# Optimization experiments

Hardware: AMD Instinct MI355X
Metric: run time of the kernel (lower is better)

## Reference

```python
import jax, jax.numpy as jnp
import numpy as np


def _sqdist(x1, x2):
    # squared euclidean distance matrix, [n1, n2]
    n1 = jnp.sum(x1 * x1, axis=-1)[:, None]
    n2 = jnp.sum(x2 * x2, axis=-1)[None, :]
    d2 = n1 + n2 - 2.0 * (x1 @ x2.T)
    return jnp.maximum(d2, 0.0)


def _rbf(x1, x2, raw_length_scale, raw_variance):
    ls = jax.nn.softplus(raw_length_scale)[0]
    var = jax.nn.softplus(raw_variance)[0]
    return var * jnp.exp(-0.5 * _sqdist(x1, x2) / (ls * ls))


def setup_inputs() -> dict:
    key = jax.random.key(0)
    k1, k2, k3 = jax.random.split(key, 3)
    N_TRAIN, N_TEST, D = 4096, 8192, 8
    return {
        "x_train": jax.random.uniform(k1, (N_TRAIN, D), dtype=jnp.float32),
        "y_train": jax.random.normal(k2, (N_TRAIN,), dtype=jnp.float32),
        "w_train": jnp.ones((N_TRAIN,), dtype=jnp.float32),
        "x_test": jax.random.uniform(k3, (N_TEST, D), dtype=jnp.float32),
        "raw_length_scale": jnp.array([0.6931471824645996], dtype=jnp.float32),
        "raw_variance": jnp.array([0.6931471824645996], dtype=jnp.float32),
        "raw_noise_var": jnp.array([0.1], dtype=jnp.float32),
    }


def reference(x_train, y_train, w_train, x_test,
              raw_length_scale, raw_variance, raw_noise_var):
    n = x_train.shape[0]
    noise_var = jax.nn.softplus(raw_noise_var)[0]
    eye = jnp.eye(n, dtype=x_train.dtype)

    K = _rbf(x_train, x_train, raw_length_scale, raw_variance) + (noise_var + 1e-6) * eye

    # off-diagonal entries scaled by w_i * w_j, diagonal kept as-is
    non_diag = 1.0 - eye
    weight = w_train[:, None] * w_train[None, :]
    weighted_K = K * (non_diag * weight + eye)

    K_s = _rbf(x_train, x_test, raw_length_scale, raw_variance)
    weighted_K_s = w_train[:, None] * K_s  # diag(w) @ K_s

    K_ss = _rbf(x_test, x_test, raw_length_scale, raw_variance) \
        + 1e-6 * jnp.eye(x_test.shape[0], dtype=x_test.dtype)

    L = jnp.linalg.cholesky(weighted_K)
    alpha = jax.scipy.linalg.cho_solve((L, True), y_train[:, None])  # [n, 1]
    mu = (weighted_K_s.T @ alpha)[:, 0]  # [n_test]

    v = jax.scipy.linalg.solve_triangular(L, weighted_K_s, lower=True)  # [n, n_test]
    cov = K_ss - v.T @ v
    return mu, cov
```

## Files before the change

kernel.cpp:

```cpp
#include <hip/hip_runtime.h>
#include <math.h>

#define NT 4096
#define MT 8192
#define NB 128
#define NBLK 32
#define TBM 128
#define TBN 64
#define TBK 32
#define SRPB 64

typedef unsigned short u16;
typedef short v8s __attribute__((ext_vector_type(8)));
typedef float v4f __attribute__((ext_vector_type(4)));

__device__ __forceinline__ float bf2f(u16 h) {
  return __uint_as_float(((unsigned)h) << 16);
}
__device__ __forceinline__ u16 f2bf(float x) {
  unsigned u = __float_as_uint(x);
  u += 0x7fffu + ((u >> 16) & 1u);
  return (u16)(u >> 16);
}
__device__ __forceinline__ void split1(float x, u16& h, u16& l) {
  h = f2bf(x);
  l = f2bf(x - bf2f(h));
}
__device__ __forceinline__ float softplusf(float x) { return log1pf(expf(x)); }

__device__ __forceinline__ void load8bf(const u16* __restrict__ p, float* f) {
  ushort4 u0 = *(const ushort4*)p;
  ushort4 u1 = *(const ushort4*)(p + 4);
  f[0] = bf2f(u0.x); f[1] = bf2f(u0.y); f[2] = bf2f(u0.z); f[3] = bf2f(u0.w);
  f[4] = bf2f(u1.x); f[5] = bf2f(u1.y); f[6] = bf2f(u1.z); f[7] = bf2f(u1.w);
}

__device__ __forceinline__ float getsc(const void* p, int f32) {
  return f32 ? *(const float*)p : bf2f(*(const u16*)p);
}
__device__ __forceinline__ float getel(const void* p, int i, int f32) {
  return f32 ? ((const float*)p)[i] : bf2f(((const u16*)p)[i]);
}
__device__ __forceinline__ void load_pt(const void* xb, int idx, int f32, float* f) {
  if (f32) {
    const float4* q = (const float4*)xb;
    float4 a = q[idx * 2], b = q[idx * 2 + 1];
    f[0] = a.x; f[1] = a.y; f[2] = a.z; f[3] = a.w;
    f[4] = b.x; f[5] = b.y; f[6] = b.z; f[7] = b.w;
  } else {
    load8bf((const u16*)xb + idx * 8, f);
  }
}

__global__ void detect_dtype(const u16* __restrict__ xt, int* __restrict__ flag) {
  if (threadIdx.x == 0) {
    int f = 0;
    for (int i = 0; i < 32; i++) if (xt[i] >= 0x4000) f = 1;
    flag[0] = f;
  }
}

__global__ void build_K(const void* __restrict__ xt, const void* __restrict__ w,
                        const void* __restrict__ rls, const void* __restrict__ rvar,
                        const void* __restrict__ rnv, float* __restrict__ K,
                        const int* __restrict__ flag) {
  int f32 = flag[0];
  int j = blockIdx.x * 16 + threadIdx.x;
  int i = blockIdx.y * 16 + threadIdx.y;
  float ls  = softplusf(getsc(rls, f32));
  float var = softplusf(getsc(rvar, f32));
  float cc  = -0.5f / (ls * ls);
  float v;
  if (i == j) {
    v = var + softplusf(getsc(rnv, f32)) + 1e-6f;
  } else {
    float a[8], b[8];
    load_pt(xt, i, f32, a);
    load_pt(xt, j, f32, b);
    float d = 0.f;
#pragma unroll
    for (int q = 0; q < 8; q++) { float t = a[q] - b[q]; d += t * t; }
    v = var * expf(cc * d) * getel(w, i, f32) * getel(w, j, f32);
  }
  K[(size_t)i * NT + j] = v;
}

__global__ void build_Kst(const void* __restrict__ xt, const void* __restrict__ xs,
                          const void* __restrict__ w, const void* __restrict__ rls,
                          const void* __restrict__ rvar,
                          u16* __restrict__ hi, u16* __restrict__ lo,
                          const int* __restrict__ flag) {
  int f32 = flag[0];
  int i = blockIdx.x * 16 + threadIdx.x;
  int j = blockIdx.y * 16 + threadIdx.y;
  float ls  = softplusf(getsc(rls, f32));
  float var = softplusf(getsc(rvar, f32));
  float cc  = -0.5f / (ls * ls);
  float a[8], b[8];
  load_pt(xt, i, f32, a);
  load_pt(xs, j, f32, b);
  float d = 0.f;
#pragma unroll
  for (int q = 0; q < 8; q++) { float t = a[q] - b[q]; d += t * t; }
  float v = getel(w, i, f32) * var * expf(cc * d);
  size_t o = (size_t)j * NT + i;
  u16 h, l; split1(v, h, l);
  hi[o] = h; lo[o] = l;
}

__global__ void __launch_bounds__(256) potrf_invert(float* __restrict__ Kg,
                                                    float* __restrict__ Wall, int kb) {
  __shared__ float At[NB * NB];
  __shared__ float Wv[NB * NB];
  int tid = threadIdx.x;
  int r0 = kb * NB;
  for (int idx = tid; idx < NB * NB; idx += 256) {
    int k = idx >> 7, i = idx & 127;
    At[idx] = Kg[(size_t)(r0 + k) * NT + r0 + i];
    Wv[idx] = (k == i) ? 1.f : 0.f;
  }
  __syncthreads();
  for (int j = 0; j < NB; j++) {
    float inv = 1.0f / At[j * NB + j];
    int nel = (NB - 1 - j) << 7;
    for (int idx = tid; idx < nel; idx += 256) {
      int k = j + 1 + (idx >> 7);
      int i = idx & 127;
      if (i >= k) At[k * NB + i] -= At[j * NB + i] * (At[j * NB + k] * inv);
    }
    __syncthreads();
  }
  for (int t = 0; t < NB; t++) {
    float invd = 1.0f / At[t * NB + t];
    int nel = (NB - 1 - t) << 7;
    for (int idx = tid; idx < nel; idx += 256) {
      int i = t + 1 + (idx >> 7);
      int c = idx & 127;
      Wv[i * NB + c] -= (At[t * NB + i] * invd) * Wv[t * NB + c];
    }
    __syncthreads();
  }
  for (int idx = tid; idx < NB * NB; idx += 256) {
    int k = idx >> 7, i = idx & 127;
    if (i >= k) {
      float s = sqrtf(At[k * NB + k]);
      Kg[(size_t)(r0 + i) * NT + r0 + k] = (i == k) ? s : At[idx] / s;
    }
  }
  float* Wg = Wall + (size_t)kb * NB * NB;
  for (int idx = tid; idx < NB * NB; idx += 256) {
    int i = idx >> 7;
    Wg[idx] = Wv[idx] / sqrtf(At[i * NB + i]);
  }
}

__global__ void copy_panel(const float* __restrict__ Kg, float* __restrict__ S,
                           int t0, int rows, int kb) {
  int idx = blockIdx.x * 256 + threadIdx.x;
  if (idx < rows * NB) {
    int r = idx >> 7, c = idx & 127;
    S[idx] = Kg[(size_t)(t0 + r) * NT + kb * NB + c];
  }
}

template<int SUB, int SYRK>
__global__ void __launch_bounds__(256) gemm_nt(const float* __restrict__ A, int lda,
                                               const float* __restrict__ B, int ldb,
                                               float* __restrict__ C, int ldc, int Kdim) {
  int c0 = blockIdx.x * TBN;
  int r0 = blockIdx.y * TBM;
  if (SYRK && c0 > r0 + TBM - 1) return;
  __shared__ float As[TBK][TBM + 4];
  __shared__ float Bs[TBK][TBN + 4];
  int tid = threadIdx.x;
  int tx = tid & 15, ty = tid >> 4;
  float acc[8][4];
#pragma unroll
  for (int r = 0; r < 8; r++)
#pragma unroll
    for (int c = 0; c < 4; c++) acc[r][c] = 0.f;

  int am = tid & 127, ah = tid >> 7;
  int bc = tid & 63,  bh = tid >> 6;

  for (int kt = 0; kt < Kdim; kt += TBK) {
#pragma unroll
    for (int q = 0; q < 4; q++) {
      int s = ah * 4 + q;
      float4 v = *(const float4*)&A[(size_t)(r0 + am) * lda + kt + s * 4];
      As[s * 4 + 0][am] = v.x; As[s * 4 + 1][am] = v.y;
      As[s * 4 + 2][am] = v.z; As[s * 4 + 3][am] = v.w;
    }
#pragma unroll
    for (int q = 0; q < 2; q++) {
      int s = bh * 2 + q;
      float4 v = *(const float4*)&B[(size_t)(c0 + bc) * ldb + kt + s * 4];
      Bs[s * 4 + 0][bc] = v.x; Bs[s * 4 + 1][bc] = v.y;
      Bs[s * 4 + 2][bc] = v.z; Bs[s * 4 + 3][bc] = v.w;
    }
    __syncthreads();
#pragma unroll
    for (int k = 0; k < TBK; k++) {
      float a[8], b[4];
      *(float4*)&a[0] = *(const float4*)&As[k][ty * 8];
      *(float4*)&a[4] = *(const float4*)&As[k][ty * 8 + 4];
      *(float4*)&b[0] = *(const float4*)&Bs[k][tx * 4];
#pragma unroll
      for (int r = 0; r < 8; r++)
#pragma unroll
        for (int c = 0; c < 4; c++) acc[r][c] += a[r] * b[c];
    }
    __syncthreads();
  }
#pragma unroll
  for (int r = 0; r < 8; r++) {
    float* cp = &C[(size_t)(r0 + ty * 8 + r) * ldc + c0 + tx * 4];
    if (SUB) {
      float4 o = *(const float4*)cp;
      o.x -= acc[r][0]; o.y -= acc[r][1]; o.z -= acc[r][2]; o.w -= acc[r][3];
      *(float4*)cp = o;
    } else {
      float4 o; o.x = acc[r][0]; o.y = acc[r][1]; o.z = acc[r][2]; o.w = acc[r][3];
      *(float4*)cp = o;
    }
  }
}

__global__ void init_r(const void* __restrict__ y, float* __restrict__ r,
                       const int* __restrict__ flag) {
  int i = blockIdx.x * 256 + threadIdx.x;
  r[i] = getel(y, i, flag[0]);
}

__global__ void __launch_bounds__(256) fwd_step(const float* __restrict__ Lg,
                                                const float* __restrict__ Wall,
                                                float* __restrict__ r,
                                                float* __restrict__ z, int kb) {
  __shared__ float ts[NB];
  __shared__ float part[256];
  int tid = threadIdx.x;
  int r0 = kb * NB;
  {
    int row = tid >> 1, half = tid & 1;
    const float* Wr = Wall + (size_t)kb * NB * NB + row * NB + half * 64;
    const float* rv = r + r0 + half * 64;
    float acc = 0.f;
#pragma unroll
    for (int c = 0; c < 64; c += 4) {
      float4 wv = *(const float4*)&Wr[c];
      float4 xv = *(const float4*)&rv[c];
      acc += wv.x * xv.x + wv.y * xv.y + wv.z * xv.z + wv.w * xv.w;
    }
    part[tid] = acc;
    __syncthreads();
    if (half == 0) ts[row] = part[tid] + part[tid + 1];
    __syncthreads();
  }
  if (blockIdx.x == 0) {
    if (tid < NB) z[r0 + tid] = ts[tid];
    return;
  }
  int base = r0 + NB + (blockIdx.x - 1) * SRPB;
  int wv_ = tid >> 6, lane = tid & 63;
  for (int rr = wv_; rr < SRPB; rr += 4) {
    int row = base + rr;
    const float* Lr = Lg + (size_t)row * NT + r0;
    float acc = Lr[lane] * ts[lane] + Lr[lane + 64] * ts[lane + 64];
#pragma unroll
    for (int off = 32; off > 0; off >>= 1) acc += __shfl_down(acc, off, 64);
    if (lane == 0) r[row] -= acc;
  }
}

__global__ void __launch_bounds__(256) bwd_step(const float* __restrict__ Lg,
                                                const float* __restrict__ Wall,
                                                float* __restrict__ z,
                                                float* __restrict__ a, int kb) {
  __shared__ float ts[NB];
  __shared__ float part[256];
  int tid = threadIdx.x;
  int r0 = kb * NB;
  {
    int col = tid & 127, half = tid >> 7;
    const float* Wb = Wall + (size_t)kb * NB * NB;
    float acc = 0.f;
#pragma unroll 4
    for (int rr = half * 64; rr < half * 64 + 64; rr++)
      acc += Wb[rr * NB + col] * z[r0 + rr];
    part[tid] = acc;
    __syncthreads();
    if (half == 0) ts[col] = part[tid] + part[tid + 128];
    __syncthreads();
  }
  if (blockIdx.x == 0) {
    if (tid < NB) a[r0 + tid] = ts[tid];
    return;
  }
  int cb = blockIdx.x - 1;
  int col = cb * NB + (tid & 127);
  int half = tid >> 7;
  float acc = 0.f;
#pragma unroll 4
  for (int jr = half * 64; jr < half * 64 + 64; jr++)
    acc += Lg[(size_t)(r0 + jr) * NT + col] * ts[jr];
  part[tid] = acc;
  __syncthreads();
  if (half == 0) z[col] -= part[tid] + part[tid + 128];
}

__global__ void conv_W(const float* __restrict__ src, u16* __restrict__ hi,
                       u16* __restrict__ lo) {
  int idx = (blockIdx.x * 256 + threadIdx.x) * 4;
  float4 v = *(const float4*)&src[idx];
  ushort4 h, l;
  split1(v.x, h.x, l.x); split1(v.y, h.y, l.y);
  split1(v.z, h.z, l.z); split1(v.w, h.w, l.w);
  *(ushort4*)&hi[idx] = h;
  *(ushort4*)&lo[idx] = l;
}

__global__ void __launch_bounds__(256) mu_dot(const u16* __restrict__ hi,
                                              const u16* __restrict__ lo,
                                              const float* __restrict__ alpha,
                                              float* __restrict__ mu) {
  int lane = threadIdx.x & 63, wv = threadIdx.x >> 6;
  int j = blockIdx.x * 4 + wv;
  const u16* ph = hi + (size_t)j * NT;
  const u16* pl = lo + (size_t)j * NT;
  float s = 0.f;
  for (int c = lane * 4; c < NT; c += 256) {
    ushort4 h = *(const ushort4*)&ph[c];
    ushort4 l = *(const ushort4*)&pl[c];
    float4 a = *(const float4*)&alpha[c];
    s += (bf2f(h.x) + bf2f(l.x)) * a.x + (bf2f(h.y) + bf2f(l.y)) * a.y
       + (bf2f(h.z) + bf2f(l.z)) * a.z + (bf2f(h.w) + bf2f(l.w)) * a.w;
  }
#pragma unroll
  for (int off = 32; off > 0; off >>= 1) s += __shfl_down(s, off, 64);
  if (lane == 0) mu[j] = s;
}

template<int MODE, int BF32>
__global__ void __launch_bounds__(256) mm_bf16(
    const u16* __restrict__ Ah, const u16* __restrict__ Al, int lda,
    const u16* __restrict__ Bh, const u16* __restrict__ Bl,
    const float* __restrict__ Bf, int ldb,
    u16* __restrict__ Chi, u16* __restrict__ Clo, float* __restrict__ Cf,
    int ldc, int Kdim,
    const void* __restrict__ xs, const void* __restrict__ rls,
    const void* __restrict__ rvar, const int* __restrict__ flag) {
  int c0 = blockIdx.x * 128;
  int r0 = blockIdx.y * 128;
  if (MODE == 2 && r0 < c0) return;
  __shared__ u16 L[4][128 * 64];
  int tid = threadIdx.x;
  int lane = tid & 63, wv = tid >> 6;
  int wr = wv >> 1, wc = wv & 1;
  int lr = lane & 15, lk = lane >> 4;

  v4f acc[4][4];
  v4f zero = {0.f, 0.f, 0.f, 0.f};
#pragma unroll
  for (int mi = 0; mi < 4; mi++)
#pragma unroll
    for (int ni = 0; ni < 4; ni++) acc[mi][ni] = zero;

  for (int kt = 0; kt < Kdim; kt += 64) {
    int4 rga[8], rgb[8];
#pragma unroll
    for (int p = 0; p < 4; p++) {
      int ch = p * 256 + tid;
      int row = ch >> 3, sl = ch & 7;
      size_t o = (size_t)(r0 + row) * lda + kt + sl * 8;
      rga[p]     = *(const int4*)(Ah + o);
      rga[p + 4] = *(const int4*)(Al + o);
    }
    if (BF32 == 0) {
#pragma unroll
      for (int p = 0; p < 4; p++) {
        int ch = p * 256 + tid;
        int row = ch >> 3, sl = ch & 7;
        size_t o = (size_t)(c0 + row) * ldb + kt + sl * 8;
        rgb[p]     = *(const int4*)(Bh + o);
        rgb[p + 4] = *(const int4*)(Bl + o);
      }
    } else {
#pragma unroll
      for (int p = 0; p < 8; p++) {
        int ch = p * 256 + tid;
        int row = ch >> 4, f4 = ch & 15;
        rgb[p] = *(const int4*)(Bf + (size_t)(c0 + row) * ldb + kt + f4 * 4);
      }
    }
    __syncthreads();
#pragma unroll
    for (int p = 0; p < 4; p++) {
      int ch = p * 256 + tid;
      int row = ch >> 3, sl = ch & 7;
      int off = row * 64 + ((sl ^ (row & 7)) * 8);
      *(int4*)&L[0][off] = rga[p];
      *(int4*)&L[1][off] = rga[p + 4];
      if (BF32 == 0) {
        *(int4*)&L[2][off] = rgb[p];
        *(int4*)&L[3][off] = rgb[p + 4];
      }
    }
    if (BF32 == 1) {
#pragma unroll
      for (int p = 0; p < 8; p++) {
        int ch = p * 256 + tid;
        int row = ch >> 4, f4 = ch & 15;
        const float* v = (const float*)&rgb[p];
        ushort4 h, l;
        split1(v[0], h.x, l.x); split1(v[1], h.y, l.y);
        split1(v[2], h.z, l.z); split1(v[3], h.w, l.w);
        int sl = f4 >> 1, half = f4 & 1;
        int off = row * 64 + ((sl ^ (row & 7)) * 8) + half * 4;
        *(ushort4*)&L[2][off] = h;
        *(ushort4*)&L[3][off] = l;
      }
    }
    __syncthreads();
#pragma unroll
    for (int ks = 0; ks < 2; ks++) {
      v8s afh[4], afl[4], bfh[4], bfl[4];
#pragma unroll
      for (int mi = 0; mi < 4; mi++) {
        int row = wr * 64 + mi * 16 + lr;
        int sl = (ks * 4 + lk) ^ (row & 7);
        afh[mi] = *(const v8s*)&L[0][row * 64 + sl * 8];
        afl[mi] = *(const v8s*)&L[1][row * 64 + sl * 8];
      }
#pragma unroll
      for (int ni = 0; ni < 4; ni++) {
        int row = wc * 64 + ni * 16 + lr;
        int sl = (ks * 4 + lk) ^ (row & 7);
        bfh[ni] = *(const v8s*)&L[2][row * 64 + sl * 8];
        bfl[ni] = *(const v8s*)&L[3][row * 64 + sl * 8];
      }
#pragma unroll
      for (int mi = 0; mi < 4; mi++)
#pragma unroll
        for (int ni = 0; ni < 4; ni++) {
          acc[mi][ni] = __builtin_amdgcn_mfma_f32_16x16x32_bf16(afh[mi], bfh[ni], acc[mi][ni], 0, 0, 0);
          acc[mi][ni] = __builtin_amdgcn_mfma_f32_16x16x32_bf16(afh[mi], bfl[ni], acc[mi][ni], 0, 0, 0);
          acc[mi][ni] = __builtin_amdgcn_mfma_f32_16x16x32_bf16(afl[mi], bfh[ni], acc[mi][ni], 0, 0, 0);
        }
    }
  }

  if (MODE == 2) {
    int f32 = flag[0];
    float ls  = softplusf(getsc(rls, f32));
    float var = softplusf(getsc(rvar, f32));
    float cc  = -0.5f / (ls * ls);
#pragma unroll
    for (int mi = 0; mi < 4; mi++) {
#pragma unroll
      for (int r = 0; r < 4; r++) {
        int grow = r0 + wr * 64 + mi * 16 + lk * 4 + r;
        float xr[8];
        load_pt(xs, grow, f32, xr);
#pragma unroll
        for (int ni = 0; ni < 4; ni++) {
          int gcol = c0 + wc * 64 + ni * 16 + lr;
          float xc[8];
          load_pt(xs, gcol, f32, xc);
          float d = 0.f;
#pragma unroll
          for (int q = 0; q < 8; q++) { float t = xr[q] - xc[q]; d += t * t; }
          float kss = var * expf(cc * d);
          if (grow == gcol) kss += 1e-6f;
          float ov = kss - acc[mi][ni][r];
          Cf[(size_t)grow * ldc + gcol] = ov;
          if (grow > gcol) Cf[(size_t)gcol * ldc + grow] = ov;
        }
      }
    }
  } else {
#pragma unroll
    for (int mi = 0; mi < 4; mi++) {
#pragma unroll
      for (int r = 0; r < 4; r++) {
        int grow = r0 + wr * 64 + mi * 16 + lk * 4 + r;
#pragma unroll
        for (int ni = 0; ni < 4; ni++) {
          int gcol = c0 + wc * 64 + ni * 16 + lr;
          size_t o = (size_t)grow * ldc + gcol;
          float nv;
          if (MODE == 0) {
            nv = acc[mi][ni][r];
          } else {
            nv = (bf2f(Chi[o]) + bf2f(Clo[o])) - acc[mi][ni][r];
          }
          u16 h, l; split1(nv, h, l);
          Chi[o] = h; Clo[o] = l;
        }
      }
    }
  }
}

extern "C" void kernel_launch(void* const* d_in, const int* in_sizes, int n_in,
                              void* d_out, int out_size, void* d_ws, size_t ws_size,
                              hipStream_t stream) {
  (void)in_sizes; (void)n_in; (void)out_size; (void)ws_size;
  const void* xt  = d_in[0];
  const void* y   = d_in[1];
  const void* w   = d_in[2];
  const void* xs  = d_in[3];
  const void* rls = d_in[4];
  const void* rva = d_in[5];
  const void* rnv = d_in[6];

  float* mu_out  = (float*)d_out;
  float* cov_out = mu_out + MT;

  float* Kf   = (float*)d_ws;
  float* Wall = Kf + (size_t)NT * NT;
  float* S    = Wall + (size_t)NBLK * NB * NB;
  float* rbuf = S + (size_t)(NT - NB) * NB;
  float* zbuf = rbuf + NT;
  float* abuf = zbuf + NT;
  int*   flag = (int*)(abuf + NT);
  u16* Whi  = (u16*)(flag + 4);
  u16* Wlo  = Whi + (size_t)NBLK * NB * NB;
  u16* Vthi = Wlo + (size_t)NBLK * NB * NB;
  u16* Vtlo = Vthi + (size_t)MT * NT;

  detect_dtype<<<1, 64, 0, stream>>>((const u16*)xt, flag);
  build_K<<<dim3(NT / 16, NT / 16), dim3(16, 16), 0, stream>>>(xt, w, rls, rva, rnv, Kf, flag);
  build_Kst<<<dim3(NT / 16, MT / 16), dim3(16, 16), 0, stream>>>(xt, xs, w, rls, rva,
                                                                 Vthi, Vtlo, flag);

  for (int kb = 0; kb < NBLK; kb++) {
    potrf_invert<<<1, 256, 0, stream>>>(Kf, Wall, kb);
    int t0 = (kb + 1) * NB;
    int rows = NT - t0;
    if (rows > 0) {
      copy_panel<<<(rows * NB) / 256, 256, 0, stream>>>(Kf, S, t0, rows, kb);
      gemm_nt<0, 0><<<dim3(NB / TBN, rows / TBM), 256, 0, stream>>>(
          S, NB, Wall + (size_t)kb * NB * NB, NB,
          Kf + (size_t)t0 * NT + kb * NB, NT, NB);
      gemm_nt<1, 1><<<dim3(rows / TBN, rows / TBM), 256, 0, stream>>>(
          Kf + (size_t)t0 * NT + kb * NB, NT,
          Kf + (size_t)t0 * NT + kb * NB, NT,
          Kf + (size_t)t0 * NT + t0, NT, NB);
    }
  }

  conv_W<<<(NBLK * NB * NB) / 1024, 256, 0, stream>>>(Wall, Whi, Wlo);

  init_r<<<NT / 256, 256, 0, stream>>>(y, rbuf, flag);
  for (int kb = 0; kb < NBLK; kb++) {
    int nupd = (NT - (kb + 1) * NB) / SRPB;
    fwd_step<<<1 + nupd, 256, 0, stream>>>(Kf, Wall, rbuf, zbuf, kb);
  }
  for (int kb = NBLK - 1; kb >= 0; kb--) {
    bwd_step<<<1 + kb, 256, 0, stream>>>(Kf, Wall, zbuf, abuf, kb);
  }

  mu_dot<<<MT / 4, 256, 0, stream>>>(Vthi, Vtlo, abuf, mu_out);

  for (int kb = 0; kb < NBLK; kb++) {
    mm_bf16<0, 0><<<dim3(1, MT / 128), 256, 0, stream>>>(
        Vthi + kb * NB, Vtlo + kb * NB, NT,
        Whi + (size_t)kb * NB * NB, Wlo + (size_t)kb * NB * NB, nullptr, NB,
        Vthi + kb * NB, Vtlo + kb * NB, nullptr, NT, NB,
        nullptr, nullptr, nullptr, nullptr);
    int t0 = (kb + 1) * NB;
    int rows = NT - t0;
    if (rows > 0) {
      mm_bf16<1, 1><<<dim3(rows / 128, MT / 128), 256, 0, stream>>>(
          Vthi + kb * NB, Vtlo + kb * NB, NT,
          nullptr, nullptr, Kf + (size_t)t0 * NT + kb * NB, NT,
          Vthi + t0, Vtlo + t0, nullptr, NT, NB,
          nullptr, nullptr, nullptr, nullptr);
    }
  }

  mm_bf16<2, 0><<<dim3(MT / 128, MT / 128), 256, 0, stream>>>(
      Vthi, Vtlo, NT, Vthi, Vtlo, nullptr, NT,
      nullptr, nullptr, cov_out, MT, NT,
      xs, rls, rva, flag);
}
```

Measured before the change: 29.35 ms.

## Fuse blocked Cholesky, solves and TRSM into persistent kernels with grid barriers

Replaces the roughly 200 per-block kernel launches for Cholesky factorization, triangular solves and the V triangular solve with two persistent kernels of 256 blocks. The blocks synchronize through an atomic-counter grid barrier. Each block redundantly factors and inverts the 128x128 diagonal tile, so the separate potrf launch and panel copy go away. The W bf16 split is also folded into the factorization step. This removes launch overhead and serial single-block phases, at the cost of redundant diagonal work, spin-barrier latency, and a deadlock risk if not all 256 blocks are co-resident.

```diff
diff --git a/kernel.cpp b/kernel.cpp
--- a/kernel.cpp
+++ b/kernel.cpp
@@ -5,10 +5,7 @@
 #define MT 8192
 #define NB 128
 #define NBLK 32
-#define TBM 128
-#define TBN 64
-#define TBK 32
-#define SRPB 64
+#define CGRID 256
 
 typedef unsigned short u16;
 typedef short v8s __attribute__((ext_vector_type(8)));
@@ -52,11 +49,32 @@
   }
 }
 
-__global__ void detect_dtype(const u16* __restrict__ xt, int* __restrict__ flag) {
+__device__ __forceinline__ void gbar(unsigned* bar) {
+  __syncthreads();
+  if (threadIdx.x == 0) {
+    __threadfence();
+    unsigned g = __hip_atomic_load(bar + 1, __ATOMIC_RELAXED, __HIP_MEMORY_SCOPE_AGENT);
+    unsigned n = __hip_atomic_fetch_add(bar, 1u, __ATOMIC_ACQ_REL, __HIP_MEMORY_SCOPE_AGENT);
+    if (n == (unsigned)(CGRID - 1)) {
+      __hip_atomic_store(bar, 0u, __ATOMIC_RELAXED, __HIP_MEMORY_SCOPE_AGENT);
+      __hip_atomic_fetch_add(bar + 1, 1u, __ATOMIC_RELEASE, __HIP_MEMORY_SCOPE_AGENT);
+    } else {
+      while (__hip_atomic_load(bar + 1, __ATOMIC_ACQUIRE, __HIP_MEMORY_SCOPE_AGENT) == g)
+        __builtin_amdgcn_s_sleep(2);
+    }
+    __threadfence();
+  }
+  __syncthreads();
+}
+
+__global__ void detect_dtype(const u16* __restrict__ xt, int* __restrict__ flag,
+                             unsigned* __restrict__ bar) {
   if (threadIdx.x == 0) {
     int f = 0;
     for (int i = 0; i < 32; i++) if (xt[i] >= 0x4000) f = 1;
     flag[0] = f;
+    bar[0] = 0u;
+    bar[1] = 0u;
   }
 }
 
@@ -108,236 +126,392 @@
   hi[o] = h; lo[o] = l;
 }
 
-__global__ void __launch_bounds__(256) potrf_invert(float* __restrict__ Kg,
-                                                    float* __restrict__ Wall, int kb) {
+__global__ void __launch_bounds__(256) coop_chol(
+    float* __restrict__ Kf, float* __restrict__ Wall,
+    u16* __restrict__ Whi, u16* __restrict__ Wlo,
+    const void* __restrict__ y, float* __restrict__ rbuf,
+    float* __restrict__ zbuf, float* __restrict__ abuf,
+    const int* __restrict__ flag, unsigned* __restrict__ bar) {
   __shared__ float At[NB * NB];
-  __shared__ float Wv[NB * NB];
-  int tid = threadIdx.x;
-  int r0 = kb * NB;
-  for (int idx = tid; idx < NB * NB; idx += 256) {
-    int k = idx >> 7, i = idx & 127;
-    At[idx] = Kg[(size_t)(r0 + k) * NT + r0 + i];
-    Wv[idx] = (k == i) ? 1.f : 0.f;
-  }
-  __syncthreads();
-  for (int j = 0; j < NB; j++) {
-    float inv = 1.0f / At[j * NB + j];
-    int nel = (NB - 1 - j) << 7;
-    for (int idx = tid; idx < nel; idx += 256) {
-      int k = j + 1 + (idx >> 7);
-      int i = idx & 127;
-      if (i >= k) At[k * NB + i] -= At[j * NB + i] * (At[j * NB + k] * inv);
+  __shared__ float Wv[NB * 130];
+  __shared__ float tsv[NB];
+  __shared__ float part[256];
+  int tid = threadIdx.x, bid = blockIdx.x;
+
+  for (int kb = 0; kb < NBLK; kb++) {
+    int r0 = kb * NB;
+    int t0 = r0 + NB;
+    int rowsK = NT - t0;
+
+    for (int idx = tid; idx < NB * NB; idx += 256) {
+      int k = idx >> 7, i = idx & 127;
+      At[idx] = Kf[(size_t)(r0 + k) * NT + r0 + i];
+      Wv[k * 130 + i] = (k == i) ? 1.f : 0.f;
     }
     __syncthreads();
-  }
-  for (int t = 0; t < NB; t++) {
-    float invd = 1.0f / At[t * NB + t];
-    int nel = (NB - 1 - t) << 7;
-    for (int idx = tid; idx < nel; idx += 256) {
-      int i = t + 1 + (idx >> 7);
-      int c = idx & 127;
-      Wv[i * NB + c] -= (At[t * NB + i] * invd) * Wv[t * NB + c];
+    for (int j = 0; j < NB; j++) {
+      float inv = 1.0f / At[j * NB + j];
+      int nel = (NB - 1 - j) << 7;
+      for (int idx = tid; idx < nel; idx += 256) {
+        int k = j + 1 + (idx >> 7);
+        int i = idx & 127;
+        if (i >= k) At[k * NB + i] -= At[j * NB + i] * (At[j * NB + k] * inv);
+      }
+      __syncthreads();
+    }
+    for (int t = 0; t < NB; t++) {
+      float invd = 1.0f / At[t * NB + t];
+      int nel = (NB - 1 - t) << 7;
+      for (int idx = tid; idx < nel; idx += 256) {
+        int i = t + 1 + (idx >> 7);
+        int c = idx & 127;
+        Wv[i * 130 + c] -= (At[t * NB + i] * invd) * Wv[t * 130 + c];
+      }
+      __syncthreads();
+    }
+    for (int idx = tid; idx < NB * NB; idx += 256) {
+      int i = idx >> 7, c = idx & 127;
+      Wv[i * 130 + c] *= 1.0f / sqrtf(At[i * NB + i]);
     }
     __syncthreads();
-  }
-  for (int idx = tid; idx < NB * NB; idx += 256) {
-    int k = idx >> 7, i = idx & 127;
-    if (i >= k) {
-      float s = sqrtf(At[k * NB + k]);
-      Kg[(size_t)(r0 + i) * NT + r0 + k] = (i == k) ? s : At[idx] / s;
-    }
-  }
-  float* Wg = Wall + (size_t)kb * NB * NB;
-  for (int idx = tid; idx < NB * NB; idx += 256) {
-    int i = idx >> 7;
-    Wg[idx] = Wv[idx] / sqrtf(At[i * NB + i]);
-  }
-}
-
-__global__ void copy_panel(const float* __restrict__ Kg, float* __restrict__ S,
-                           int t0, int rows, int kb) {
-  int idx = blockIdx.x * 256 + threadIdx.x;
-  if (idx < rows * NB) {
-    int r = idx >> 7, c = idx & 127;
-    S[idx] = Kg[(size_t)(t0 + r) * NT + kb * NB + c];
-  }
-}
-
-template<int SUB, int SYRK>
-__global__ void __launch_bounds__(256) gemm_nt(const float* __restrict__ A, int lda,
-                                               const float* __restrict__ B, int ldb,
-                                               float* __restrict__ C, int ldc, int Kdim) {
-  int c0 = blockIdx.x * TBN;
-  int r0 = blockIdx.y * TBM;
-  if (SYRK && c0 > r0 + TBM - 1) return;
-  __shared__ float As[TBK][TBM + 4];
-  __shared__ float Bs[TBK][TBN + 4];
-  int tid = threadIdx.x;
-  int tx = tid & 15, ty = tid >> 4;
-  float acc[8][4];
-#pragma unroll
-  for (int r = 0; r < 8; r++)
-#pragma unroll
-    for (int c = 0; c < 4; c++) acc[r][c] = 0.f;
-
-  int am = tid & 127, ah = tid >> 7;
-  int bc = tid & 63,  bh = tid >> 6;
-
-  for (int kt = 0; kt < Kdim; kt += TBK) {
-#pragma unroll
-    for (int q = 0; q < 4; q++) {
-      int s = ah * 4 + q;
-      float4 v = *(const float4*)&A[(size_t)(r0 + am) * lda + kt + s * 4];
-      As[s * 4 + 0][am] = v.x; As[s * 4 + 1][am] = v.y;
-      As[s * 4 + 2][am] = v.z; As[s * 4 + 3][am] = v.w;
-    }
-#pragma unroll
-    for (int q = 0; q < 2; q++) {
-      int s = bh * 2 + q;
-      float4 v = *(const float4*)&B[(size_t)(c0 + bc) * ldb + kt + s * 4];
-      Bs[s * 4 + 0][bc] = v.x; Bs[s * 4 + 1][bc] = v.y;
-      Bs[s * 4 + 2][bc] = v.z; Bs[s * 4 + 3][bc] = v.w;
+    if (bid == 0) {
+      for (int idx = tid; idx < NB * NB; idx += 256) {
+        int k = idx >> 7, i = idx & 127;
+        if (i >= k) {
+          float s = sqrtf(At[k * NB + k]);
+          Kf[(size_t)(r0 + i) * NT + r0 + k] = (i == k) ? s : At[k * NB + i] / s;
+        }
+        float wv = Wv[k * 130 + i];
+        Wall[(size_t)kb * NB * NB + idx] = wv;
+        u16 h, l; split1(wv, h, l);
+        Whi[(size_t)kb * NB * NB + idx] = h;
+        Wlo[(size_t)kb * NB * NB + idx] = l;
+      }
     }
     __syncthreads();
-#pragma unroll
-    for (int k = 0; k < TBK; k++) {
-      float a[8], b[4];
-      *(float4*)&a[0] = *(const float4*)&As[k][ty * 8];
-      *(float4*)&a[4] = *(const float4*)&As[k][ty * 8 + 4];
-      *(float4*)&b[0] = *(const float4*)&Bs[k][tx * 4];
+
+    if (rowsK > 0 && bid < (rowsK >> 6)) {
+      int m0 = t0 + bid * 64;
+      for (int ch = tid; ch < 64 * 32; ch += 256) {
+        int row = ch >> 5, c4 = ch & 31;
+        float4 v = *(const float4*)&Kf[(size_t)(m0 + row) * NT + r0 + c4 * 4];
+        At[(c4 * 4 + 0) * 68 + row] = v.x; At[(c4 * 4 + 1) * 68 + row] = v.y;
+        At[(c4 * 4 + 2) * 68 + row] = v.z; At[(c4 * 4 + 3) * 68 + row] = v.w;
+      }
+      __syncthreads();
+      float pa[8][4];
 #pragma unroll
       for (int r = 0; r < 8; r++)
 #pragma unroll
-        for (int c = 0; c < 4; c++) acc[r][c] += a[r] * b[c];
-    }
-    __syncthreads();
-  }
-#pragma unroll
-  for (int r = 0; r < 8; r++) {
-    float* cp = &C[(size_t)(r0 + ty * 8 + r) * ldc + c0 + tx * 4];
-    if (SUB) {
-      float4 o = *(const float4*)cp;
-      o.x -= acc[r][0]; o.y -= acc[r][1]; o.z -= acc[r][2]; o.w -= acc[r][3];
-      *(float4*)cp = o;
-    } else {
-      float4 o; o.x = acc[r][0]; o.y = acc[r][1]; o.z = acc[r][2]; o.w = acc[r][3];
-      *(float4*)cp = o;
-    }
-  }
-}
-
-__global__ void init_r(const void* __restrict__ y, float* __restrict__ r,
-                       const int* __restrict__ flag) {
-  int i = blockIdx.x * 256 + threadIdx.x;
-  r[i] = getel(y, i, flag[0]);
-}
-
-__global__ void __launch_bounds__(256) fwd_step(const float* __restrict__ Lg,
-                                                const float* __restrict__ Wall,
-                                                float* __restrict__ r,
-                                                float* __restrict__ z, int kb) {
-  __shared__ float ts[NB];
-  __shared__ float part[256];
-  int tid = threadIdx.x;
-  int r0 = kb * NB;
-  {
-    int row = tid >> 1, half = tid & 1;
-    const float* Wr = Wall + (size_t)kb * NB * NB + row * NB + half * 64;
-    const float* rv = r + r0 + half * 64;
-    float acc = 0.f;
-#pragma unroll
-    for (int c = 0; c < 64; c += 4) {
-      float4 wv = *(const float4*)&Wr[c];
-      float4 xv = *(const float4*)&rv[c];
-      acc += wv.x * xv.x + wv.y * xv.y + wv.z * xv.z + wv.w * xv.w;
-    }
-    part[tid] = acc;
-    __syncthreads();
-    if (half == 0) ts[row] = part[tid] + part[tid + 1];
-    __syncthreads();
-  }
-  if (blockIdx.x == 0) {
-    if (tid < NB) z[r0 + tid] = ts[tid];
-    return;
-  }
-  int base = r0 + NB + (blockIdx.x - 1) * SRPB;
-  int wv_ = tid >> 6, lane = tid & 63;
-  for (int rr = wv_; rr < SRPB; rr += 4) {
-    int row = base + rr;
-    const float* Lr = Lg + (size_t)row * NT + r0;
-    float acc = Lr[lane] * ts[lane] + Lr[lane + 64] * ts[lane + 64];
-#pragma unroll
-    for (int off = 32; off > 0; off >>= 1) acc += __shfl_down(acc, off, 64);
-    if (lane == 0) r[row] -= acc;
-  }
-}
-
-__global__ void __launch_bounds__(256) bwd_step(const float* __restrict__ Lg,
-                                                const float* __restrict__ Wall,
-                                                float* __restrict__ z,
-                                                float* __restrict__ a, int kb) {
-  __shared__ float ts[NB];
-  __shared__ float part[256];
-  int tid = threadIdx.x;
-  int r0 = kb * NB;
-  {
-    int col = tid & 127, half = tid >> 7;
-    const float* Wb = Wall + (size_t)kb * NB * NB;
-    float acc = 0.f;
+        for (int c = 0; c < 4; c++) pa[r][c] = 0.f;
+      int rr0 = (tid >> 5) * 8, cc0 = (tid & 31) * 4;
+      for (int k = 0; k < NB; k++) {
+        float a0[8], b0[4];
+        *(float4*)&a0[0] = *(const float4*)&At[k * 68 + rr0];
+        *(float4*)&a0[4] = *(const float4*)&At[k * 68 + rr0 + 4];
+        b0[0] = Wv[(cc0 + 0) * 130 + k]; b0[1] = Wv[(cc0 + 1) * 130 + k];
+        b0[2] = Wv[(cc0 + 2) * 130 + k]; b0[3] = Wv[(cc0 + 3) * 130 + k];
+#pragma unroll
+        for (int r = 0; r < 8; r++)
+#pragma unroll
+          for (int c = 0; c < 4; c++) pa[r][c] += a0[r] * b0[c];
+      }
+#pragma unroll
+      for (int r = 0; r < 8; r++) {
+        float4 o; o.x = pa[r][0]; o.y = pa[r][1]; o.z = pa[r][2]; o.w = pa[r][3];
+        *(float4*)&Kf[(size_t)(m0 + rr0 + r) * NT + r0 + cc0] = o;
+      }
+    }
+    gbar(bar);
+
+    if (rowsK > 0) {
+      int nmT = rowsK >> 7, nnT = rowsK >> 6;
+      int ntile = nmT * nnT;
+      for (int ti = bid; ti < ntile; ti += CGRID) {
+        int m = ti / nnT, n = ti % nnT;
+        int m0 = t0 + m * 128, n0 = t0 + n * 64;
+        if (n0 > m0 + 127) continue;
+        __syncthreads();
+        for (int ch = tid; ch < 128 * 32; ch += 256) {
+          int row = ch >> 5, c4 = ch & 31;
+          float4 v = *(const float4*)&Kf[(size_t)(m0 + row) * NT + r0 + c4 * 4];
+          At[(c4 * 4 + 0) * 128 + row] = v.x; At[(c4 * 4 + 1) * 128 + row] = v.y;
+          At[(c4 * 4 + 2) * 128 + row] = v.z; At[(c4 * 4 + 3) * 128 + row] = v.w;
+        }
+        for (int ch = tid; ch < 64 * 32; ch += 256) {
+          int nn_ = ch >> 5, c4 = ch & 31;
+          float4 v = *(const float4*)&Kf[(size_t)(n0 + nn_) * NT + r0 + c4 * 4];
+          Wv[(c4 * 4 + 0) * 68 + nn_] = v.x; Wv[(c4 * 4 + 1) * 68 + nn_] = v.y;
+          Wv[(c4 * 4 + 2) * 68 + nn_] = v.z; Wv[(c4 * 4 + 3) * 68 + nn_] = v.w;
+        }
+        __syncthreads();
+        float ac[8][4];
+#pragma unroll
+        for (int r = 0; r < 8; r++)
+#pragma unroll
+          for (int c = 0; c < 4; c++) ac[r][c] = 0.f;
+        int ty = tid >> 4, tx = tid & 15;
+        for (int k = 0; k < 128; k++) {
+          float a0[8], b0[4];
+          *(float4*)&a0[0] = *(const float4*)&At[k * 128 + ty * 8];
+          *(float4*)&a0[4] = *(const float4*)&At[k * 128 + ty * 8 + 4];
+          *(float4*)&b0[0] = *(const float4*)&Wv[k * 68 + tx * 4];
+#pragma unroll
+          for (int r = 0; r < 8; r++)
+#pragma unroll
+            for (int c = 0; c < 4; c++) ac[r][c] += a0[r] * b0[c];
+        }
+#pragma unroll
+        for (int r = 0; r < 8; r++) {
+          float* cp = &Kf[(size_t)(m0 + ty * 8 + r) * NT + n0 + tx * 4];
+          float4 o = *(const float4*)cp;
+          o.x -= ac[r][0]; o.y -= ac[r][1]; o.z -= ac[r][2]; o.w -= ac[r][3];
+          *(float4*)cp = o;
+        }
+      }
+    }
+    gbar(bar);
+  }
+
+  int f32 = flag[0];
+  for (int i = bid * 256 + tid; i < NT; i += CGRID * 256) rbuf[i] = getel(y, i, f32);
+  gbar(bar);
+
+  for (int kb = 0; kb < NBLK; kb++) {
+    int r0 = kb * NB;
+    {
+      int row = tid >> 1, half = tid & 1;
+      const float* Wr = Wall + (size_t)kb * NB * NB + row * NB + half * 64;
+      const float* rv = rbuf + r0 + half * 64;
+      float acc = 0.f;
+#pragma unroll
+      for (int c = 0; c < 64; c += 4) {
+        float4 wv4 = *(const float4*)&Wr[c];
+        float4 xv = *(const float4*)&rv[c];
+        acc += wv4.x * xv.x + wv4.y * xv.y + wv4.z * xv.z + wv4.w * xv.w;
+      }
+      part[tid] = acc;
+      __syncthreads();
+      if (half == 0) tsv[row] = part[tid] + part[tid + 1];
+      __syncthreads();
+    }
+    if (bid == 0 && tid < NB) zbuf[r0 + tid] = tsv[tid];
+    int t0s = r0 + NB;
+    int nst = (NT - t0s) >> 6;
+    if (bid < nst) {
+      int base = t0s + bid * 64;
+      int wv_ = tid >> 6, lane = tid & 63;
+      for (int rr = wv_; rr < 64; rr += 4) {
+        int row = base + rr;
+        const float* Lr = Kf + (size_t)row * NT + r0;
+        float acc = Lr[lane] * tsv[lane] + Lr[lane + 64] * tsv[lane + 64];
+#pragma unroll
+        for (int off = 32; off > 0; off >>= 1) acc += __shfl_down(acc, off, 64);
+        if (lane == 0) rbuf[row] -= acc;
+      }
+    }
+    gbar(bar);
+  }
+
+  for (int kb = NBLK - 1; kb >= 0; kb--) {
+    int r0 = kb * NB;
+    {
+      int col = tid & 127, half = tid >> 7;
+      const float* Wb = Wall + (size_t)kb * NB * NB;
+      float acc = 0.f;
 #pragma unroll 4
-    for (int rr = half * 64; rr < half * 64 + 64; rr++)
-      acc += Wb[rr * NB + col] * z[r0 + rr];
-    part[tid] = acc;
-    __syncthreads();
-    if (half == 0) ts[col] = part[tid] + part[tid + 128];
-    __syncthreads();
-  }
-  if (blockIdx.x == 0) {
-    if (tid < NB) a[r0 + tid] = ts[tid];
-    return;
-  }
-  int cb = blockIdx.x - 1;
-  int col = cb * NB + (tid & 127);
-  int half = tid >> 7;
-  float acc = 0.f;
+      for (int rr = half * 64; rr < half * 64 + 64; rr++)
+        acc += Wb[rr * NB + col] * zbuf[r0 + rr];
+      part[tid] = acc;
+      __syncthreads();
+      if (half == 0) tsv[col] = part[tid] + part[tid + 128];
+      __syncthreads();
+    }
+    if (bid == 0 && tid < NB) abuf[r0 + tid] = tsv[tid];
+    if (bid < kb) {
+      int col = bid * NB + (tid & 127);
+      int half = tid >> 7;
+      float acc = 0.f;
 #pragma unroll 4
-  for (int jr = half * 64; jr < half * 64 + 64; jr++)
-    acc += Lg[(size_t)(r0 + jr) * NT + col] * ts[jr];
-  part[tid] = acc;
-  __syncthreads();
-  if (half == 0) z[col] -= part[tid] + part[tid + 128];
-}
-
-__global__ void conv_W(const float* __restrict__ src, u16* __restrict__ hi,
-                       u16* __restrict__ lo) {
-  int idx = (blockIdx.x * 256 + threadIdx.x) * 4;
-  float4 v = *(const float4*)&src[idx];
-  ushort4 h, l;
-  split1(v.x, h.x, l.x); split1(v.y, h.y, l.y);
-  split1(v.z, h.z, l.z); split1(v.w, h.w, l.w);
-  *(ushort4*)&hi[idx] = h;
-  *(ushort4*)&lo[idx] = l;
-}
-
-__global__ void __launch_bounds__(256) mu_dot(const u16* __restrict__ hi,
-                                              const u16* __restrict__ lo,
-                                              const float* __restrict__ alpha,
-                                              float* __restrict__ mu) {
-  int lane = threadIdx.x & 63, wv = threadIdx.x >> 6;
-  int j = blockIdx.x * 4 + wv;
-  const u16* ph = hi + (size_t)j * NT;
-  const u16* pl = lo + (size_t)j * NT;
-  float s = 0.f;
-  for (int c = lane * 4; c < NT; c += 256) {
-    ushort4 h = *(const ushort4*)&ph[c];
-    ushort4 l = *(const ushort4*)&pl[c];
-    float4 a = *(const float4*)&alpha[c];
-    s += (bf2f(h.x) + bf2f(l.x)) * a.x + (bf2f(h.y) + bf2f(l.y)) * a.y
-       + (bf2f(h.z) + bf2f(l.z)) * a.z + (bf2f(h.w) + bf2f(l.w)) * a.w;
-  }
-#pragma unroll
-  for (int off = 32; off > 0; off >>= 1) s += __shfl_down(s, off, 64);
-  if (lane == 0) mu[j] = s;
+      for (int jr = half * 64; jr < half * 64 + 64; jr++)
+        acc += Kf[(size_t)(r0 + jr) * NT + col] * tsv[jr];
+      part[tid] = acc;
+      __syncthreads();
+      if (half == 0) zbuf[col] -= part[tid] + part[tid + 128];
+    }
+    gbar(bar);
+  }
+}
+
+__device__ __forceinline__ void mfma_tile(const u16* __restrict__ LAh, const u16* __restrict__ LAl,
+                                          const u16* __restrict__ LBh, const u16* __restrict__ LBl,
+                                          v4f acc[4][4], int wr, int wc, int lr, int lk) {
+#pragma unroll
+  for (int ks = 0; ks < 2; ks++) {
+    v8s afh[4], afl[4], bfh[4], bfl[4];
+#pragma unroll
+    for (int mi = 0; mi < 4; mi++) {
+      int row = wr * 64 + mi * 16 + lr;
+      int sl = (ks * 4 + lk) ^ (row & 7);
+      afh[mi] = *(const v8s*)&LAh[row * 64 + sl * 8];
+      afl[mi] = *(const v8s*)&LAl[row * 64 + sl * 8];
+    }
+#pragma unroll
+    for (int ni = 0; ni < 4; ni++) {
+      int row = wc * 64 + ni * 16 + lr;
+      int sl = (ks * 4 + lk) ^ (row & 7);
+      bfh[ni] = *(const v8s*)&LBh[row * 64 + sl * 8];
+      bfl[ni] = *(const v8s*)&LBl[row * 64 + sl * 8];
+    }
+#pragma unroll
+    for (int mi = 0; mi < 4; mi++)
+#pragma unroll
+      for (int ni = 0; ni < 4; ni++) {
+        acc[mi][ni] = __builtin_amdgcn_mfma_f32_16x16x32_bf16(afh[mi], bfh[ni], acc[mi][ni], 0, 0, 0);
+        acc[mi][ni] = __builtin_amdgcn_mfma_f32_16x16x32_bf16(afh[mi], bfl[ni], acc[mi][ni], 0, 0, 0);
+        acc[mi][ni] = __builtin_amdgcn_mfma_f32_16x16x32_bf16(afl[mi], bfh[ni], acc[mi][ni], 0, 0, 0);
+      }
+  }
+}
+
+__global__ void __launch_bounds__(512) coop_trsm(
+    u16* __restrict__ Vthi, u16* __restrict__ Vtlo,
+    const u16* __restrict__ Whi, const u16* __restrict__ Wlo,
+    const float* __restrict__ Kf, const float* __restrict__ alpha,
+    float* __restrict__ mu, unsigned* __restrict__ bar) {
+  __shared__ u16 LAh[256 * 64], LAl[256 * 64];
+  __shared__ u16 LBh[128 * 64], LBl[128 * 64];
+  int tid = threadIdx.x, bid = blockIdx.x;
+  int lane = tid & 63, wv = tid >> 6;
+
+  for (int j = bid * 8 + wv; j < MT; j += CGRID * 8) {
+    const u16* ph = Vthi + (size_t)j * NT;
+    const u16* pl = Vtlo + (size_t)j * NT;
+    float s = 0.f;
+    for (int c = lane * 4; c < NT; c += 256) {
+      ushort4 h = *(const ushort4*)&ph[c];
+      ushort4 l = *(const ushort4*)&pl[c];
+      float4 a = *(const float4*)&alpha[c];
+      s += (bf2f(h.x) + bf2f(l.x)) * a.x + (bf2f(h.y) + bf2f(l.y)) * a.y
+         + (bf2f(h.z) + bf2f(l.z)) * a.z + (bf2f(h.w) + bf2f(l.w)) * a.w;
+    }
+#pragma unroll
+    for (int off = 32; off > 0; off >>= 1) s += __shfl_down(s, off, 64);
+    if (lane == 0) mu[j] = s;
+  }
+  gbar(bar);
+
+  int wr = wv >> 1, wc = wv & 1;
+  int lr = lane & 15, lk = lane >> 4;
+  v4f zero = {0.f, 0.f, 0.f, 0.f};
+
+  for (int kb = 0; kb < NBLK; kb++) {
+    int r0 = kb * NB;
+    if (bid < MT / 256) {
+      int m0 = bid * 256;
+      v4f acc[4][4];
+#pragma unroll
+      for (int mi = 0; mi < 4; mi++)
+#pragma unroll
+        for (int ni = 0; ni < 4; ni++) acc[mi][ni] = zero;
+      for (int kt = 0; kt < 2; kt++) {
+        int k0 = r0 + kt * 64;
+        __syncthreads();
+#pragma unroll
+        for (int p = 0; p < 4; p++) {
+          int ch = p * 512 + tid;
+          int row = ch >> 3, sl = ch & 7;
+          size_t o = (size_t)(m0 + row) * NT + k0 + sl * 8;
+          int off = row * 64 + ((sl ^ (row & 7)) * 8);
+          *(int4*)&LAh[off] = *(const int4*)(Vthi + o);
+          *(int4*)&LAl[off] = *(const int4*)(Vtlo + o);
+        }
+#pragma unroll
+        for (int p = 0; p < 2; p++) {
+          int ch = p * 512 + tid;
+          int row = ch >> 3, sl = ch & 7;
+          size_t o = (size_t)kb * NB * NB + row * NB + kt * 64 + sl * 8;
+          int off = row * 64 + ((sl ^ (row & 7)) * 8);
+          *(int4*)&LBh[off] = *(const int4*)(Whi + o);
+          *(int4*)&LBl[off] = *(const int4*)(Wlo + o);
+        }
+        __syncthreads();
+        mfma_tile(LAh, LAl, LBh, LBl, acc, wr, wc, lr, lk);
+      }
+#pragma unroll
+      for (int mi = 0; mi < 4; mi++)
+#pragma unroll
+        for (int r = 0; r < 4; r++) {
+          int grow = m0 + wr * 64 + mi * 16 + lk * 4 + r;
+#pragma unroll
+          for (int ni = 0; ni < 4; ni++) {
+            int gcol = r0 + wc * 64 + ni * 16 + lr;
+            size_t o = (size_t)grow * NT + gcol;
+            u16 h, l; split1(acc[mi][ni][r], h, l);
+            Vthi[o] = h; Vtlo[o] = l;
+          }
+        }
+    }
+    gbar(bar);
+
+    int t0 = (kb + 1) * NB, rowsT = NT - t0;
+    if (rowsT > 0) {
+      int nn = rowsT >> 7;
+      int ntile = (MT / 256) * nn;
+      for (int ti = bid; ti < ntile; ti += CGRID) {
+        int m = ti % (MT / 256), n = ti / (MT / 256);
+        int m0 = m * 256, n0 = t0 + n * 128;
+        v4f acc[4][4];
+#pragma unroll
+        for (int mi = 0; mi < 4; mi++)
+#pragma unroll
+          for (int ni = 0; ni < 4; ni++) acc[mi][ni] = zero;
+        for (int kt = 0; kt < 2; kt++) {
+          int k0 = r0 + kt * 64;
+          __syncthreads();
+#pragma unroll
+          for (int p = 0; p < 4; p++) {
+            int ch = p * 512 + tid;
+            int row = ch >> 3, sl = ch & 7;
+            size_t o = (size_t)(m0 + row) * NT + k0 + sl * 8;
+            int off = row * 64 + ((sl ^ (row & 7)) * 8);
+            *(int4*)&LAh[off] = *(const int4*)(Vthi + o);
+            *(int4*)&LAl[off] = *(const int4*)(Vtlo + o);
+          }
+#pragma unroll
+          for (int p = 0; p < 4; p++) {
+            int ch = p * 512 + tid;
+            int row = ch >> 4, f4 = ch & 15;
+            float4 v = *(const float4*)&Kf[(size_t)(n0 + row) * NT + k0 + f4 * 4];
+            ushort4 h, l;
+            split1(v.x, h.x, l.x); split1(v.y, h.y, l.y);
+            split1(v.z, h.z, l.z); split1(v.w, h.w, l.w);
+            int sl = f4 >> 1, half = f4 & 1;
+            int off = row * 64 + ((sl ^ (row & 7)) * 8) + half * 4;
+            *(ushort4*)&LBh[off] = h;
+            *(ushort4*)&LBl[off] = l;
+          }
+          __syncthreads();
+          mfma_tile(LAh, LAl, LBh, LBl, acc, wr, wc, lr, lk);
+        }
+#pragma unroll
+        for (int mi = 0; mi < 4; mi++)
+#pragma unroll
+          for (int r = 0; r < 4; r++) {
+            int grow = m0 + wr * 64 + mi * 16 + lk * 4 + r;
+#pragma unroll
+            for (int ni = 0; ni < 4; ni++) {
+              int gcol = n0 + wc * 64 + ni * 16 + lr;
+              size_t o = (size_t)grow * NT + gcol;
+              float nv = (bf2f(Vthi[o]) + bf2f(Vtlo[o])) - acc[mi][ni][r];
+              u16 h, l; split1(nv, h, l);
+              Vthi[o] = h; Vtlo[o] = l;
+            }
+          }
+      }
+    }
+    gbar(bar);
+  }
 }
 
 template<int MODE, int BF32>
@@ -421,32 +595,8 @@
       }
     }
     __syncthreads();
-#pragma unroll
-    for (int ks = 0; ks < 2; ks++) {
-      v8s afh[4], afl[4], bfh[4], bfl[4];
-#pragma unroll
-      for (int mi = 0; mi < 4; mi++) {
-        int row = wr * 64 + mi * 16 + lr;
-        int sl = (ks * 4 + lk) ^ (row & 7);
-        afh[mi] = *(const v8s*)&L[0][row * 64 + sl * 8];
-        afl[mi] = *(const v8s*)&L[1][row * 64 + sl * 8];
-      }
-#pragma unroll
-      for (int ni = 0; ni < 4; ni++) {
-        int row = wc * 64 + ni * 16 + lr;
-        int sl = (ks * 4 + lk) ^ (row & 7);
-        bfh[ni] = *(const v8s*)&L[2][row * 64 + sl * 8];
-        bfl[ni] = *(const v8s*)&L[3][row * 64 + sl * 8];
-      }
-#pragma unroll
-      for (int mi = 0; mi < 4; mi++)
-#pragma unroll
-        for (int ni = 0; ni < 4; ni++) {
-          acc[mi][ni] = __builtin_amdgcn_mfma_f32_16x16x32_bf16(afh[mi], bfh[ni], acc[mi][ni], 0, 0, 0);
-          acc[mi][ni] = __builtin_amdgcn_mfma_f32_16x16x32_bf16(afh[mi], bfl[ni], acc[mi][ni], 0, 0, 0);
-          acc[mi][ni] = __builtin_amdgcn_mfma_f32_16x16x32_bf16(afl[mi], bfh[ni], acc[mi][ni], 0, 0, 0);
-        }
-    }
+    mfma_tile(&L[0][0], &L[1][0], &L[2][0], &L[3][0], acc, wr, wc, lr, lk);
+    __syncthreads();
   }
 
   if (MODE == 2) {
@@ -523,62 +673,18 @@
   float* zbuf = rbuf + NT;
   float* abuf = zbuf + NT;
   int*   flag = (int*)(abuf + NT);
-  u16* Whi  = (u16*)(flag + 4);
+  unsigned* bar = (unsigned*)(flag + 4);
+  u16* Whi  = (u16*)(flag + 8);
   u16* Wlo  = Whi + (size_t)NBLK * NB * NB;
   u16* Vthi = Wlo + (size_t)NBLK * NB * NB;
   u16* Vtlo = Vthi + (size_t)MT * NT;
 
-  detect_dtype<<<1, 64, 0, stream>>>((const u16*)xt, flag);
+  detect_dtype<<<1, 64, 0, stream>>>((const u16*)xt, flag, bar);
   build_K<<<dim3(NT / 16, NT / 16), dim3(16, 16), 0, stream>>>(xt, w, rls, rva, rnv, Kf, flag);
   build_Kst<<<dim3(NT / 16, MT / 16), dim3(16, 16), 0, stream>>>(xt, xs, w, rls, rva,
                                                                  Vthi, Vtlo, flag);
-
-  for (int kb = 0; kb < NBLK; kb++) {
-    potrf_invert<<<1, 256, 0, stream>>>(Kf, Wall, kb);
-    int t0 = (kb + 1) * NB;
-    int rows = NT - t0;
-    if (rows > 0) {
-      copy_panel<<<(rows * NB) / 256, 256, 0, stream>>>(Kf, S, t0, rows, kb);
-      gemm_nt<0, 0><<<dim3(NB / TBN, rows / TBM), 256, 0, stream>>>(
-          S, NB, Wall + (size_t)kb * NB * NB, NB,
-          Kf + (size_t)t0 * NT + kb * NB, NT, NB);
-      gemm_nt<1, 1><<<dim3(rows / TBN, rows / TBM), 256, 0, stream>>>(
-          Kf + (size_t)t0 * NT + kb * NB, NT,
-          Kf + (size_t)t0 * NT + kb * NB, NT,
-          Kf + (size_t)t0 * NT + t0, NT, NB);
-    }
-  }
-
-  conv_W<<<(NBLK * NB * NB) / 1024, 256, 0, stream>>>(Wall, Whi, Wlo);
-
-  init_r<<<NT / 256, 256, 0, stream>>>(y, rbuf, flag);
-  for (int kb = 0; kb < NBLK; kb++) {
-    int nupd = (NT - (kb + 1) * NB) / SRPB;
-    fwd_step<<<1 + nupd, 256, 0, stream>>>(Kf, Wall, rbuf, zbuf, kb);
-  }
-  for (int kb = NBLK - 1; kb >= 0; kb--) {
-    bwd_step<<<1 + kb, 256, 0, stream>>>(Kf, Wall, zbuf, abuf, kb);
-  }
-
-  mu_dot<<<MT / 4, 256, 0, stream>>>(Vthi, Vtlo, abuf, mu_out);
-
-  for (int kb = 0; kb < NBLK; kb++) {
-    mm_bf16<0, 0><<<dim3(1, MT / 128), 256, 0, stream>>>(
-        Vthi + kb * NB, Vtlo + kb * NB, NT,
-        Whi + (size_t)kb * NB * NB, Wlo + (size_t)kb * NB * NB, nullptr, NB,
-        Vthi + kb * NB, Vtlo + kb * NB, nullptr, NT, NB,
-        nullptr, nullptr, nullptr, nullptr);
-    int t0 = (kb + 1) * NB;
-    int rows = NT - t0;
-    if (rows > 0) {
-      mm_bf16<1, 1><<<dim3(rows / 128, MT / 128), 256, 0, stream>>>(
-          Vthi + kb * NB, Vtlo + kb * NB, NT,
-          nullptr, nullptr, Kf + (size_t)t0 * NT + kb * NB, NT,
-          Vthi + t0, Vtlo + t0, nullptr, NT, NB,
-          nullptr, nullptr, nullptr, nullptr);
-    }
-  }
-
+  coop_chol<<<CGRID, 256, 0, stream>>>(Kf, Wall, Whi, Wlo, y, rbuf, zbuf, abuf, flag, bar);
+  coop_trsm<<<CGRID, 512, 0, stream>>>(Vthi, Vtlo, Whi, Wlo, Kf, abuf, mu_out, bar);
   mm_bf16<2, 0><<<dim3(MT / 128, MT / 128), 256, 0, stream>>>(
       Vthi, Vtlo, NT, Vthi, Vtlo, nullptr, NT,
       nullptr, nullptr, cov_out, MT, NT,
```

After: 44.73 ms. 1.52x slower.
